# Kernel tuning notes

Hardware: AMD Instinct MI355X
Metric: run time of the kernel (lower is better)

## Reference

```python
import jax, jax.numpy as jnp
import numpy as np

N, F, K, D = 4096, 512, 8, 64


def setup_inputs() -> dict:
    key = jax.random.key(0)
    ks = jax.random.split(key, 6)
    H = jax.random.normal(ks[0], (N, F), dtype=jnp.float32)
    # dense 0/1 adjacency with self-loops
    A = jax.random.randint(ks[1], (N, N), 0, 2).astype(jnp.float32)
    A = jnp.maximum(A, jnp.eye(N, dtype=jnp.float32))
    idx = jnp.arange(N, dtype=jnp.int64)
    glorot_w = (2.0 / (F + D)) ** 0.5
    glorot_a = (2.0 / (D + 1)) ** 0.5
    kernels = glorot_w * jax.random.normal(ks[2], (K, F, D), dtype=jnp.float32)
    attn_kernels = glorot_a * jax.random.normal(ks[3], (K, 2, D, 1), dtype=jnp.float32)
    biases = 0.01 * jax.random.normal(ks[4], (K, D), dtype=jnp.float32)
    return {"H": H, "A": A, "idx": idx, "kernels": kernels,
            "attn_kernels": attn_kernels, "biases": biases}


def reference(H, A, idx, kernels, attn_kernels, biases):
    # (dropout is identity at inference)
    batch_A = A[:, idx]                                  # [N, N]
    HW = jnp.einsum('nf,kfd->knd', H, kernels)           # [K, N, D]
    a1 = attn_kernels[:, 0, :, 0]                        # [K, D]
    a2 = attn_kernels[:, 1, :, 0]                        # [K, D]
    s1 = jnp.einsum('knd,kd->kn', HW, a1)                # score_i (source)
    s2 = jnp.einsum('knd,kd->kn', HW, a2)                # score_j (target)
    scores = s1[:, :, None] + s2[:, None, :]             # [K, N, N]
    neg_big = jnp.finfo(jnp.float32).min
    scores = jnp.where(batch_A[None, :, :] == 0.0, neg_big, scores)
    # LeakyReLU(0.2) applied AFTER masking, as in the original
    scores = jnp.where(scores >= 0, scores, 0.2 * scores)
    attn = jax.nn.softmax(scores, axis=-1)               # [K, N, N]
    res = jnp.einsum('kij,kjd->kid', attn, HW) + biases[:, None, :]  # [K, N, D]
    out = jax.nn.elu(res)                                # is_last=False -> concat heads
    out = jnp.transpose(out, (1, 0, 2)).reshape(N, K * D)
    return out
```

## Files before the change

kernel.cpp:

```cpp
#include <hip/hip_runtime.h>
#include <hip/hip_fp16.h>
#include <float.h>
#include <math.h>

#define NN 4096
#define FF 512
#define KK 8
#define DD 64

typedef float f32x4 __attribute__((ext_vector_type(4)));
typedef _Float16 h2 __attribute__((ext_vector_type(2)));
typedef _Float16 f16x4 __attribute__((ext_vector_type(4)));
typedef _Float16 f16x8 __attribute__((ext_vector_type(8)));
typedef unsigned int u32;
typedef unsigned long long u64;

__device__ __forceinline__ h2 H2(u32 u) { union { u32 u; h2 h; } x; x.u = u; return x.h; }
__device__ __forceinline__ u32 U32(h2 h) { union { u32 u; h2 h; } x; x.h = h; return x.u; }
__device__ __forceinline__ u32 pmask(u32 m, int sh) {
  u32 b = (m >> sh) & 3u;
  return ((b * 0x10001u) & 0x20001u) * 0xFFFFu;
}
__device__ __forceinline__ u32 encf(float f) {
  u32 u = __float_as_uint(f);
  return ((int)u < 0) ? ~u : (u | 0x80000000u);
}
__device__ __forceinline__ float decf(u32 e) {
  u32 u = (e & 0x80000000u) ? (e ^ 0x80000000u) : ~e;
  return __uint_as_float(u);
}

__global__ __launch_bounds__(256) void k_bits(const float* __restrict__ A,
                                              u64* __restrict__ bits,
                                              u32* __restrict__ mxu) {
  if (blockIdx.x == 0 && threadIdx.x < KK) mxu[threadIdx.x] = 0u;
  const int gw = (blockIdx.x * 256 + threadIdx.x) >> 6;
  const int lane = threadIdx.x & 63;
  const int nw = (gridDim.x * 256) >> 6;
  const int totw = NN * NN / 64;
  for (int wd = gw; wd < totw; wd += nw) {
    float a = A[(size_t)wd * 64 + lane];
    u64 m = __ballot(a != 0.0f);
    if (lane == 0) bits[wd] = m;
  }
}

__global__ __launch_bounds__(256) void k_prep(const float* __restrict__ H,
                                              const float* __restrict__ Wk,
                                              _Float16* __restrict__ HF,
                                              _Float16* __restrict__ WF) {
  const int w = threadIdx.x >> 6, lane = threadIdx.x & 63;
  const int l15 = lane & 15, grp = lane >> 4;
  if (blockIdx.x < 1024) {
    const int tile = blockIdx.x * 4 + w;
    const int rb = tile >> 4, fb = tile & 15;
    const float* src = H + (size_t)(rb * 16 + l15) * FF + fb * 32 + grp * 4;
    float4 lo = *reinterpret_cast<const float4*>(src);
    float4 hi = *reinterpret_cast<const float4*>(src + 16);
    f16x8 v;
    v[0] = (_Float16)lo.x; v[1] = (_Float16)lo.y; v[2] = (_Float16)lo.z; v[3] = (_Float16)lo.w;
    v[4] = (_Float16)hi.x; v[5] = (_Float16)hi.y; v[6] = (_Float16)hi.z; v[7] = (_Float16)hi.w;
    *reinterpret_cast<f16x8*>(HF + (size_t)tile * 512 + lane * 8) = v;
  } else {
    const int g = (blockIdx.x - 1024) * 256 + threadIdx.x;
    const int frag = g >> 6, fl = g & 63;
    const int fl15 = fl & 15, fgrp = fl >> 4;
    const int k = frag >> 6, fb = (frag >> 2) & 15, db = frag & 3;
    f16x8 v;
    #pragma unroll
    for (int e = 0; e < 8; ++e) {
      int f = fb * 32 + fgrp * 4 + (e & 3) + 16 * (e >> 2);
      int d = db * 16 + fl15;
      v[e] = (_Float16)Wk[((size_t)k * FF + f) * DD + d];
    }
    *reinterpret_cast<f16x8*>(WF + (size_t)frag * 512 + fl * 8) = v;
  }
}

__global__ __launch_bounds__(256) void k_hw(const _Float16* __restrict__ HF,
                                            const _Float16* __restrict__ WF,
                                            const float* __restrict__ attk,
                                            _Float16* __restrict__ HWF,
                                            float* __restrict__ s1,
                                            float* __restrict__ s2,
                                            u32* __restrict__ mxu) {
  __shared__ float wmax[4];
  const int w = threadIdx.x >> 6, lane = threadIdx.x & 63;
  const int k = blockIdx.y;
  const int rb = blockIdx.x * 4 + w;
  const int l15 = lane & 15, grp = lane >> 4;
  f32x4 acc[4] = {};
  const _Float16* hfb = HF + (size_t)(rb * 16) * 512 + lane * 8;
  const _Float16* wfk = WF + (size_t)k * 64 * 512 + lane * 8;
  #pragma unroll 4
  for (int fb = 0; fb < 16; ++fb) {
    f16x8 a = *reinterpret_cast<const f16x8*>(hfb + (size_t)fb * 512);
    #pragma unroll
    for (int n = 0; n < 4; ++n) {
      f16x8 b = *reinterpret_cast<const f16x8*>(wfk + (size_t)(fb * 4 + n) * 512);
      acc[n] = __builtin_amdgcn_mfma_f32_16x16x32_f16(a, b, acc[n], 0, 0, 0);
    }
  }
  const int jb = rb >> 1;
  const int half = rb & 1;
  #pragma unroll
  for (int db = 0; db < 4; ++db) {
    f16x4 v;
    #pragma unroll
    for (int q = 0; q < 4; ++q) v[q] = (_Float16)acc[db][q];
    *reinterpret_cast<f16x4*>(HWF + (size_t)((k * 128 + jb) * 4 + db) * 512 + lane * 8 + half * 4) = v;
  }
  float a1v[4], a2v[4];
  #pragma unroll
  for (int n = 0; n < 4; ++n) {
    a1v[n] = attk[k * 2 * DD + n * 16 + l15];
    a2v[n] = attk[k * 2 * DD + DD + n * 16 + l15];
  }
  float pm2 = -FLT_MAX;
  #pragma unroll
  for (int q = 0; q < 4; ++q) {
    float p1 = 0.f, p2 = 0.f;
    #pragma unroll
    for (int n = 0; n < 4; ++n) { p1 += acc[n][q] * a1v[n]; p2 += acc[n][q] * a2v[n]; }
    #pragma unroll
    for (int off = 8; off; off >>= 1) { p1 += __shfl_xor(p1, off); p2 += __shfl_xor(p2, off); }
    if (l15 == 0) {
      int row = rb * 16 + grp * 4 + q;
      s1[k * NN + row] = p1;
      s2[k * NN + row] = p2;
    }
    pm2 = fmaxf(pm2, p2);
  }
  pm2 = fmaxf(pm2, __shfl_xor(pm2, 16));
  pm2 = fmaxf(pm2, __shfl_xor(pm2, 32));
  if (lane == 0) wmax[w] = pm2;
  __syncthreads();
  if (threadIdx.x == 0) {
    float bm = fmaxf(fmaxf(wmax[0], wmax[1]), fmaxf(wmax[2], wmax[3]));
    atomicMax(&mxu[k], encf(bm));
  }
}

__global__ __launch_bounds__(256, 2) void k_attn(
    const u64* __restrict__ bits, const _Float16* __restrict__ HWF,
    const float* __restrict__ s1, const float* __restrict__ s2,
    const u32* __restrict__ mxu, const float* __restrict__ bias,
    float* __restrict__ out) {
  __shared__ __align__(16) _Float16 epl[4096];
  __shared__ __align__(16) _Float16 enl[4096];
  __shared__ _Float16 srf[2][64][72];
  __shared__ float wsl[4][64];
  __shared__ float rtot[64];
  const int k = blockIdx.y;
  const int i0 = blockIdx.x * 64;
  const int tid = threadIdx.x;
  const int w = tid >> 6, lane = tid & 63, l15 = lane & 15, grp = lane >> 4;
  const float mxk = decf(mxu[k]);
  #pragma unroll
  for (int c = 0; c < 2; ++c) {
    const int j8 = tid * 16 + c * 8;
    float4 sa = *reinterpret_cast<const float4*>(&s2[k * NN + j8]);
    float4 sb = *reinterpret_cast<const float4*>(&s2[k * NN + j8 + 4]);
    f16x4 e0, e1, n0, n1;
    e0[0] = (_Float16)__expf(sa.x - mxk); e0[1] = (_Float16)__expf(sa.y - mxk);
    e0[2] = (_Float16)__expf(sa.z - mxk); e0[3] = (_Float16)__expf(sa.w - mxk);
    e1[0] = (_Float16)__expf(sb.x - mxk); e1[1] = (_Float16)__expf(sb.y - mxk);
    e1[2] = (_Float16)__expf(sb.z - mxk); e1[3] = (_Float16)__expf(sb.w - mxk);
    n0[0] = (_Float16)__expf(0.2f * (sa.x - mxk)); n0[1] = (_Float16)__expf(0.2f * (sa.y - mxk));
    n0[2] = (_Float16)__expf(0.2f * (sa.z - mxk)); n0[3] = (_Float16)__expf(0.2f * (sa.w - mxk));
    n1[0] = (_Float16)__expf(0.2f * (sb.x - mxk)); n1[1] = (_Float16)__expf(0.2f * (sb.y - mxk));
    n1[2] = (_Float16)__expf(0.2f * (sb.z - mxk)); n1[3] = (_Float16)__expf(0.2f * (sb.w - mxk));
    *reinterpret_cast<f16x4*>(&epl[j8])     = e0;
    *reinterpret_cast<f16x4*>(&epl[j8 + 4]) = e1;
    *reinterpret_cast<f16x4*>(&enl[j8])     = n0;
    *reinterpret_cast<f16x4*>(&enl[j8 + 4]) = n1;
  }
  h2 P1h[4], Q1h[4];
  #pragma unroll
  for (int s = 0; s < 4; ++s) {
    int row = i0 + s * 16 + l15;
    float s1r = s1[k * NN + row];
    float t = s1r + mxk;
    float cr = fmaxf(t, 0.2f * t);
    _Float16 p = (_Float16)__expf(t - cr);
    _Float16 q = (_Float16)__expf(0.2f * t - cr);
    P1h[s] = h2{p, p}; Q1h[s] = h2{q, q};
  }
  __syncthreads();
  const int g4 = grp * 4;
  const u64* br0 = bits + (size_t)(i0 + l15) * (NN / 64) + w * 16;
  const _Float16* hwb = HWF + ((size_t)(k * 128 + w * 32) * 4) * 512 + lane * 8;
  const h2 ones = h2{(_Float16)1.0f, (_Float16)1.0f};
  f32x4 acc[4][4] = {};
  float wsum[4] = {};
  for (int jw = 0; jw < 16; ++jw) {
    u64 bw[4];
    #pragma unroll
    for (int s = 0; s < 4; ++s) bw[s] = br0[jw + s * 1024];
    #pragma unroll
    for (int hf = 0; hf < 2; ++hf) {
      const int js = jw * 2 + hf;
      const int jl = w * 1024 + js * 32;
      f16x8 bf0 = *reinterpret_cast<const f16x8*>(hwb + (js * 4 + 0) * 512);
      f16x8 bf1 = *reinterpret_cast<const f16x8*>(hwb + (js * 4 + 1) * 512);
      f16x8 bf2 = *reinterpret_cast<const f16x8*>(hwb + (js * 4 + 2) * 512);
      f16x8 bf3 = *reinterpret_cast<const f16x8*>(hwb + (js * 4 + 3) * 512);
      f16x4 elo = *reinterpret_cast<const f16x4*>(&epl[jl + g4]);
      f16x4 ehi = *reinterpret_cast<const f16x4*>(&epl[jl + 16 + g4]);
      f16x4 nlo = *reinterpret_cast<const f16x4*>(&enl[jl + g4]);
      f16x4 nhi = *reinterpret_cast<const f16x4*>(&enl[jl + 16 + g4]);
      const u32 e01 = ((const u32*)&elo)[0], e23 = ((const u32*)&elo)[1];
      const u32 e45 = ((const u32*)&ehi)[0], e67 = ((const u32*)&ehi)[1];
      const u32 n01 = ((const u32*)&nlo)[0], n23 = ((const u32*)&nlo)[1];
      const u32 n45 = ((const u32*)&nhi)[0], n67 = ((const u32*)&nhi)[1];
      #pragma unroll
      for (int s = 0; s < 4; ++s) {
        const u32 m32 = (u32)(bw[s] >> (hf * 32));
        u32 p0 = U32(__builtin_elementwise_max(P1h[s] * H2(e01), Q1h[s] * H2(n01))) & pmask(m32, g4);
        u32 p1 = U32(__builtin_elementwise_max(P1h[s] * H2(e23), Q1h[s] * H2(n23))) & pmask(m32, g4 + 2);
        u32 p2 = U32(__builtin_elementwise_max(P1h[s] * H2(e45), Q1h[s] * H2(n45))) & pmask(m32, g4 + 16);
        u32 p3 = U32(__builtin_elementwise_max(P1h[s] * H2(e67), Q1h[s] * H2(n67))) & pmask(m32, g4 + 18);
        wsum[s] = __builtin_amdgcn_fdot2(H2(p0), ones, wsum[s], false);
        wsum[s] = __builtin_amdgcn_fdot2(H2(p1), ones, wsum[s], false);
        wsum[s] = __builtin_amdgcn_fdot2(H2(p2), ones, wsum[s], false);
        wsum[s] = __builtin_amdgcn_fdot2(H2(p3), ones, wsum[s], false);
        union { u32 u[4]; f16x8 v; } af;
        af.u[0] = p0; af.u[1] = p1; af.u[2] = p2; af.u[3] = p3;
        acc[s][0] = __builtin_amdgcn_mfma_f32_16x16x32_f16(af.v, bf0, acc[s][0], 0, 0, 0);
        acc[s][1] = __builtin_amdgcn_mfma_f32_16x16x32_f16(af.v, bf1, acc[s][1], 0, 0, 0);
        acc[s][2] = __builtin_amdgcn_mfma_f32_16x16x32_f16(af.v, bf2, acc[s][2], 0, 0, 0);
        acc[s][3] = __builtin_amdgcn_mfma_f32_16x16x32_f16(af.v, bf3, acc[s][3], 0, 0, 0);
      }
    }
  }
  #pragma unroll
  for (int s = 0; s < 4; ++s) {
    wsum[s] += __shfl_xor(wsum[s], 16);
    wsum[s] += __shfl_xor(wsum[s], 32);
  }
  auto store_surf = [&](int id) {
    #pragma unroll
    for (int s = 0; s < 4; ++s)
      #pragma unroll
      for (int n = 0; n < 4; ++n)
        #pragma unroll
        for (int q = 0; q < 4; ++q)
          srf[id][s * 16 + grp * 4 + q][n * 16 + l15] = (_Float16)acc[s][n][q];
  };
  auto add_surf = [&](int id) {
    #pragma unroll
    for (int s = 0; s < 4; ++s)
      #pragma unroll
      for (int n = 0; n < 4; ++n)
        #pragma unroll
        for (int q = 0; q < 4; ++q)
          acc[s][n][q] += (float)srf[id][s * 16 + grp * 4 + q][n * 16 + l15];
  };
  if (w >= 2) store_surf(w - 2);
  if (grp == 0) {
    #pragma unroll
    for (int s = 0; s < 4; ++s) wsl[w][s * 16 + l15] = wsum[s];
  }
  __syncthreads();
  if (w < 2) add_surf(w);
  if (tid < 64) {
    float t = wsl[0][tid] + wsl[1][tid] + wsl[2][tid] + wsl[3][tid];
    rtot[tid] = 1.0f / t;
  }
  __syncthreads();
  if (w == 1) store_surf(0);
  __syncthreads();
  if (w == 0) {
    add_surf(0);
    float biasv[4];
    #pragma unroll
    for (int n = 0; n < 4; ++n) biasv[n] = bias[k * DD + n * 16 + l15];
    #pragma unroll
    for (int s = 0; s < 4; ++s)
      #pragma unroll
      for (int q = 0; q < 4; ++q) {
        const int row = s * 16 + grp * 4 + q;
        const float rw = rtot[row];
        #pragma unroll
        for (int n = 0; n < 4; ++n) {
          float v = acc[s][n][q] * rw + biasv[n];
          v = v > 0.f ? v : expm1f(v);
          out[(size_t)(i0 + row) * (KK * DD) + k * DD + n * 16 + l15] = v;
        }
      }
  }
}

extern "C" void kernel_launch(void* const* d_in, const int* in_sizes, int n_in,
                              void* d_out, int out_size, void* d_ws, size_t ws_size,
                              hipStream_t stream) {
  const float* H    = (const float*)d_in[0];
  const float* A    = (const float*)d_in[1];
  const float* Wk   = (const float*)d_in[3];
  const float* attk = (const float*)d_in[4];
  const float* bias = (const float*)d_in[5];
  float* out = (float*)d_out;

  char* base = (char*)d_ws;
  _Float16* HWF = (_Float16*)(base + 0);
  _Float16* WF  = (_Float16*)(base + 4194304);
  _Float16* HF  = (_Float16*)(base + 4718592);
  u64* bits     = (u64*)(base + 8912896);
  float* s1p    = (float*)(base + 11010048);
  float* s2p    = (float*)(base + 11141120);
  u32* mxu      = (u32*)(base + 11272192);

  k_bits<<<2048, 256, 0, stream>>>(A, bits, mxu);
  k_prep<<<1152, 256, 0, stream>>>(H, Wk, HF, WF);
  k_hw<<<dim3(NN / 64, KK), 256, 0, stream>>>(HF, WF, attk, HWF, s1p, s2p, mxu);
  k_attn<<<dim3(NN / 64, KK), 256, 0, stream>>>(bits, HWF, s1p, s2p, mxu, bias, out);
}
```

Measured before the change: 176.6 us.

## Precompute exp tables in separate kernel and halve attention row tile

Moves the per-block exp(s2) table computation out of the attention kernel into a small k_tab kernel that writes fp16 tables to workspace. The attention kernel now reads those tables from global/cache instead of LDS and processes 32 rows per block instead of 64, which doubles the grid and raises occupancy to 4 blocks per SM. The cost is an extra launch, twice as many reads of HW and the bit mask per output row, and exp-table loads that now go through global memory.

Result: slower. 188.8 us (+6.9%).

```diff
diff --git a/kernel.cpp b/kernel.cpp
--- a/kernel.cpp
+++ b/kernel.cpp
@@ -141,43 +141,45 @@
   }
 }
 
-__global__ __launch_bounds__(256, 2) void k_attn(
+__global__ __launch_bounds__(256) void k_tab(const float* __restrict__ s2,
+                                             const u32* __restrict__ mxu,
+                                             _Float16* __restrict__ ep,
+                                             _Float16* __restrict__ en) {
+  const int k = blockIdx.y;
+  const float mxk = decf(mxu[k]);
+  const int j0 = (blockIdx.x * 256 + threadIdx.x) * 8;
+  float4 sa = *reinterpret_cast<const float4*>(&s2[k * NN + j0]);
+  float4 sb = *reinterpret_cast<const float4*>(&s2[k * NN + j0 + 4]);
+  f16x8 e, n;
+  e[0] = (_Float16)__expf(sa.x - mxk); e[1] = (_Float16)__expf(sa.y - mxk);
+  e[2] = (_Float16)__expf(sa.z - mxk); e[3] = (_Float16)__expf(sa.w - mxk);
+  e[4] = (_Float16)__expf(sb.x - mxk); e[5] = (_Float16)__expf(sb.y - mxk);
+  e[6] = (_Float16)__expf(sb.z - mxk); e[7] = (_Float16)__expf(sb.w - mxk);
+  n[0] = (_Float16)__expf(0.2f * (sa.x - mxk)); n[1] = (_Float16)__expf(0.2f * (sa.y - mxk));
+  n[2] = (_Float16)__expf(0.2f * (sa.z - mxk)); n[3] = (_Float16)__expf(0.2f * (sa.w - mxk));
+  n[4] = (_Float16)__expf(0.2f * (sb.x - mxk)); n[5] = (_Float16)__expf(0.2f * (sb.y - mxk));
+  n[6] = (_Float16)__expf(0.2f * (sb.z - mxk)); n[7] = (_Float16)__expf(0.2f * (sb.w - mxk));
+  *reinterpret_cast<f16x8*>(&ep[k * NN + j0]) = e;
+  *reinterpret_cast<f16x8*>(&en[k * NN + j0]) = n;
+}
+
+__global__ __launch_bounds__(256, 4) void k_attn(
     const u64* __restrict__ bits, const _Float16* __restrict__ HWF,
-    const float* __restrict__ s1, const float* __restrict__ s2,
+    const float* __restrict__ s1,
+    const _Float16* __restrict__ ep, const _Float16* __restrict__ en,
     const u32* __restrict__ mxu, const float* __restrict__ bias,
     float* __restrict__ out) {
-  __shared__ __align__(16) _Float16 epl[4096];
-  __shared__ __align__(16) _Float16 enl[4096];
-  __shared__ _Float16 srf[2][64][72];
-  __shared__ float wsl[4][64];
-  __shared__ float rtot[64];
+  __shared__ _Float16 srf[2][32][72];
+  __shared__ float wsl[4][32];
+  __shared__ float rtot[32];
   const int k = blockIdx.y;
-  const int i0 = blockIdx.x * 64;
+  const int i0 = blockIdx.x * 32;
   const int tid = threadIdx.x;
   const int w = tid >> 6, lane = tid & 63, l15 = lane & 15, grp = lane >> 4;
   const float mxk = decf(mxu[k]);
-  #pragma unroll
-  for (int c = 0; c < 2; ++c) {
-    const int j8 = tid * 16 + c * 8;
-    float4 sa = *reinterpret_cast<const float4*>(&s2[k * NN + j8]);
-    float4 sb = *reinterpret_cast<const float4*>(&s2[k * NN + j8 + 4]);
-    f16x4 e0, e1, n0, n1;
-    e0[0] = (_Float16)__expf(sa.x - mxk); e0[1] = (_Float16)__expf(sa.y - mxk);
-    e0[2] = (_Float16)__expf(sa.z - mxk); e0[3] = (_Float16)__expf(sa.w - mxk);
-    e1[0] = (_Float16)__expf(sb.x - mxk); e1[1] = (_Float16)__expf(sb.y - mxk);
-    e1[2] = (_Float16)__expf(sb.z - mxk); e1[3] = (_Float16)__expf(sb.w - mxk);
-    n0[0] = (_Float16)__expf(0.2f * (sa.x - mxk)); n0[1] = (_Float16)__expf(0.2f * (sa.y - mxk));
-    n0[2] = (_Float16)__expf(0.2f * (sa.z - mxk)); n0[3] = (_Float16)__expf(0.2f * (sa.w - mxk));
-    n1[0] = (_Float16)__expf(0.2f * (sb.x - mxk)); n1[1] = (_Float16)__expf(0.2f * (sb.y - mxk));
-    n1[2] = (_Float16)__expf(0.2f * (sb.z - mxk)); n1[3] = (_Float16)__expf(0.2f * (sb.w - mxk));
-    *reinterpret_cast<f16x4*>(&epl[j8])     = e0;
-    *reinterpret_cast<f16x4*>(&epl[j8 + 4]) = e1;
-    *reinterpret_cast<f16x4*>(&enl[j8])     = n0;
-    *reinterpret_cast<f16x4*>(&enl[j8 + 4]) = n1;
-  }
-  h2 P1h[4], Q1h[4];
-  #pragma unroll
-  for (int s = 0; s < 4; ++s) {
+  h2 P1h[2], Q1h[2];
+  #pragma unroll
+  for (int s = 0; s < 2; ++s) {
     int row = i0 + s * 16 + l15;
     float s1r = s1[k * NN + row];
     float t = s1r + mxk;
@@ -186,35 +188,36 @@
     _Float16 q = (_Float16)__expf(0.2f * t - cr);
     P1h[s] = h2{p, p}; Q1h[s] = h2{q, q};
   }
-  __syncthreads();
   const int g4 = grp * 4;
   const u64* br0 = bits + (size_t)(i0 + l15) * (NN / 64) + w * 16;
   const _Float16* hwb = HWF + ((size_t)(k * 128 + w * 32) * 4) * 512 + lane * 8;
+  const _Float16* epk = ep + (size_t)k * NN + w * 1024 + g4;
+  const _Float16* enk = en + (size_t)k * NN + w * 1024 + g4;
   const h2 ones = h2{(_Float16)1.0f, (_Float16)1.0f};
-  f32x4 acc[4][4] = {};
-  float wsum[4] = {};
+  f32x4 acc[2][4] = {};
+  float wsum[2] = {};
   for (int jw = 0; jw < 16; ++jw) {
-    u64 bw[4];
-    #pragma unroll
-    for (int s = 0; s < 4; ++s) bw[s] = br0[jw + s * 1024];
+    u64 bw[2];
+    bw[0] = br0[jw];
+    bw[1] = br0[jw + 1024];
     #pragma unroll
     for (int hf = 0; hf < 2; ++hf) {
       const int js = jw * 2 + hf;
-      const int jl = w * 1024 + js * 32;
+      const int jo = js * 32;
       f16x8 bf0 = *reinterpret_cast<const f16x8*>(hwb + (js * 4 + 0) * 512);
       f16x8 bf1 = *reinterpret_cast<const f16x8*>(hwb + (js * 4 + 1) * 512);
       f16x8 bf2 = *reinterpret_cast<const f16x8*>(hwb + (js * 4 + 2) * 512);
       f16x8 bf3 = *reinterpret_cast<const f16x8*>(hwb + (js * 4 + 3) * 512);
-      f16x4 elo = *reinterpret_cast<const f16x4*>(&epl[jl + g4]);
-      f16x4 ehi = *reinterpret_cast<const f16x4*>(&epl[jl + 16 + g4]);
-      f16x4 nlo = *reinterpret_cast<const f16x4*>(&enl[jl + g4]);
-      f16x4 nhi = *reinterpret_cast<const f16x4*>(&enl[jl + 16 + g4]);
+      f16x4 elo = *reinterpret_cast<const f16x4*>(epk + jo);
+      f16x4 ehi = *reinterpret_cast<const f16x4*>(epk + jo + 16);
+      f16x4 nlo = *reinterpret_cast<const f16x4*>(enk + jo);
+      f16x4 nhi = *reinterpret_cast<const f16x4*>(enk + jo + 16);
       const u32 e01 = ((const u32*)&elo)[0], e23 = ((const u32*)&elo)[1];
       const u32 e45 = ((const u32*)&ehi)[0], e67 = ((const u32*)&ehi)[1];
       const u32 n01 = ((const u32*)&nlo)[0], n23 = ((const u32*)&nlo)[1];
       const u32 n45 = ((const u32*)&nhi)[0], n67 = ((const u32*)&nhi)[1];
       #pragma unroll
-      for (int s = 0; s < 4; ++s) {
+      for (int s = 0; s < 2; ++s) {
         const u32 m32 = (u32)(bw[s] >> (hf * 32));
         u32 p0 = U32(__builtin_elementwise_max(P1h[s] * H2(e01), Q1h[s] * H2(n01))) & pmask(m32, g4);
         u32 p1 = U32(__builtin_elementwise_max(P1h[s] * H2(e23), Q1h[s] * H2(n23))) & pmask(m32, g4 + 2);
@@ -234,13 +237,13 @@
     }
   }
   #pragma unroll
-  for (int s = 0; s < 4; ++s) {
+  for (int s = 0; s < 2; ++s) {
     wsum[s] += __shfl_xor(wsum[s], 16);
     wsum[s] += __shfl_xor(wsum[s], 32);
   }
   auto store_surf = [&](int id) {
     #pragma unroll
-    for (int s = 0; s < 4; ++s)
+    for (int s = 0; s < 2; ++s)
       #pragma unroll
       for (int n = 0; n < 4; ++n)
         #pragma unroll
@@ -249,7 +252,7 @@
   };
   auto add_surf = [&](int id) {
     #pragma unroll
-    for (int s = 0; s < 4; ++s)
+    for (int s = 0; s < 2; ++s)
       #pragma unroll
       for (int n = 0; n < 4; ++n)
         #pragma unroll
@@ -257,13 +260,10 @@
           acc[s][n][q] += (float)srf[id][s * 16 + grp * 4 + q][n * 16 + l15];
   };
   if (w >= 2) store_surf(w - 2);
-  if (grp == 0) {
-    #pragma unroll
-    for (int s = 0; s < 4; ++s) wsl[w][s * 16 + l15] = wsum[s];
-  }
+  if (grp == 0) { wsl[w][l15] = wsum[0]; wsl[w][16 + l15] = wsum[1]; }
   __syncthreads();
   if (w < 2) add_surf(w);
-  if (tid < 64) {
+  if (tid < 32) {
     float t = wsl[0][tid] + wsl[1][tid] + wsl[2][tid] + wsl[3][tid];
     rtot[tid] = 1.0f / t;
   }
@@ -276,7 +276,7 @@
     #pragma unroll
     for (int n = 0; n < 4; ++n) biasv[n] = bias[k * DD + n * 16 + l15];
     #pragma unroll
-    for (int s = 0; s < 4; ++s)
+    for (int s = 0; s < 2; ++s)
       #pragma unroll
       for (int q = 0; q < 4; ++q) {
         const int row = s * 16 + grp * 4 + q;
@@ -309,9 +309,12 @@
   float* s1p    = (float*)(base + 11010048);
   float* s2p    = (float*)(base + 11141120);
   u32* mxu      = (u32*)(base + 11272192);
+  _Float16* epp = (_Float16*)(base + 11276288);
+  _Float16* enp = (_Float16*)(base + 11341824);
 
   k_bits<<<2048, 256, 0, stream>>>(A, bits, mxu);
   k_prep<<<1152, 256, 0, stream>>>(H, Wk, HF, WF);
   k_hw<<<dim3(NN / 64, KK), 256, 0, stream>>>(HF, WF, attk, HWF, s1p, s2p, mxu);
-  k_attn<<<dim3(NN / 64, KK), 256, 0, stream>>>(bits, HWF, s1p, s2p, mxu, bias, out);
-}
+  k_tab<<<dim3(2, KK), 256, 0, stream>>>(s2p, mxu, epp, enp);
+  k_attn<<<dim3(NN / 32, KK), 256, 0, stream>>>(bits, HWF, s1p, epp, enp, mxu, bias, out);
+}
```
